# Performance work log

Measured on AMD Instinct MI355X. Metric: run time of the kernel, lower is better.

## Reference

```python
import jax, jax.numpy as jnp
import numpy as np

EMB = 512       # emb_dim
H = 8           # n_heads
HD = EMB // H   # head_dim = 64
FREQ = 64       # freq_features
PERIOD = 0.1
N = 2048


def setup_inputs() -> dict:
    key = jax.random.key(0)
    ks = jax.random.split(key, 6)
    x = jax.random.normal(ks[0], (1, N, EMB), dtype=jnp.float32)
    v = jax.random.normal(ks[1], (1, N, 3), dtype=jnp.float32)
    vec_map = v / jnp.linalg.norm(v, axis=-1, keepdims=True)  # unit direction vectors
    s_in = 1.0 / np.sqrt(EMB)
    W_qkv = jax.random.normal(ks[2], (EMB, 3 * EMB), dtype=jnp.float32) * s_in
    b_qkv = jnp.zeros((3 * EMB,), dtype=jnp.float32)
    W_bias = jax.random.normal(ks[3], (FREQ, H), dtype=jnp.float32) * (1.0 / np.sqrt(FREQ))
    b_bias = jnp.zeros((H,), dtype=jnp.float32)
    W_out = jax.random.normal(ks[4], (EMB, EMB), dtype=jnp.float32) * s_in
    b_out = jnp.zeros((EMB,), dtype=jnp.float32)
    return {"x": x, "vec_map": vec_map, "W_qkv": W_qkv, "b_qkv": b_qkv,
            "W_bias": W_bias, "b_bias": b_bias, "W_out": W_out, "b_out": b_out}


def reference(x, vec_map, W_qkv, b_qkv, W_bias, b_bias, W_out, b_out):
    batch_dim = x.shape[:-2]
    n = x.shape[-2]
    # QKV projection -> (*, N, H, 3, HD)
    qkv = (x @ W_qkv + b_qkv).reshape(*batch_dim, n, H, 3, HD)
    q, k, v = (qkv[..., 0, :], qkv[..., 1, :], qkv[..., 2, :])
    # attention scores (*, Q, K, H), softmax over the K axis (axis=-2)
    attn = jnp.einsum('...qht,...kht->...qkh', q, k) / np.sqrt(HD)
    attn = jax.nn.softmax(attn, axis=-2)
    # relative bias from pairwise angles between direction vectors
    dot = jnp.einsum('...nc,...mc->...nm', vec_map, vec_map)
    angle = jnp.arccos(jnp.clip(dot, 0.0, 1.0)) / 0.001
    freqs = jnp.linspace(0.0, 1.0, FREQ // 2, dtype=jnp.float32) / PERIOD
    phase = freqs * angle[..., None]                      # (*, N, N, FREQ/2)
    pos = jnp.concatenate((jnp.sin(phase), jnp.cos(phase)), axis=-1)  # (*, N, N, FREQ)
    bias = pos @ W_bias + b_bias                          # (*, N, N, H)
    attn = attn + bias
    # weighted sum of values -> (*, N, EMB)
    y = jnp.einsum('...qkh,...kht->...qht', attn, v).reshape(*batch_dim, n, EMB)
    return y @ W_out + b_out
```

## Files before the change

### kernel.cpp

```cpp
#include <hip/hip_runtime.h>
#include <hip/hip_bf16.h>
#include <math.h>

#define NT 2048
#define EMBD 512
#define NH 8
#define QKV_LD 1536

typedef unsigned short u16;
typedef __attribute__((ext_vector_type(8))) short short8;
typedef __attribute__((ext_vector_type(4))) float v4f;

static __device__ __forceinline__ float bf2f(unsigned int u) {
    union { unsigned int i; float f; } c; c.i = u << 16; return c.f;
}
static __device__ __forceinline__ void unpack8(uint4 r, float* f) {
    f[0] = bf2f(r.x & 0xffffu); f[1] = bf2f(r.x >> 16);
    f[2] = bf2f(r.y & 0xffffu); f[3] = bf2f(r.y >> 16);
    f[4] = bf2f(r.z & 0xffffu); f[5] = bf2f(r.z >> 16);
    f[6] = bf2f(r.w & 0xffffu); f[7] = bf2f(r.w >> 16);
}
static __device__ __forceinline__ void unpack4(uint2 r, float* f) {
    f[0] = bf2f(r.x & 0xffffu); f[1] = bf2f(r.x >> 16);
    f[2] = bf2f(r.y & 0xffffu); f[3] = bf2f(r.y >> 16);
}
static __device__ __forceinline__ unsigned int f2bf(float x) {
    union { float f; unsigned int u; } c; c.f = x;
    return (c.u + 0x7fffu + ((c.u >> 16) & 1u)) >> 16;
}

__global__ __launch_bounds__(256) void split_x(const float* __restrict__ x,
    u16* __restrict__ xh, u16* __restrict__ xl)
{
    int i = (blockIdx.x * 256 + threadIdx.x) << 2;
    float4 v = *(const float4*)(x + i);
    float f[4] = {v.x, v.y, v.z, v.w};
    unsigned int hi[4], lo[4];
#pragma unroll
    for (int j = 0; j < 4; ++j) {
        hi[j] = f2bf(f[j]);
        lo[j] = f2bf(f[j] - bf2f(hi[j]));
    }
    uint2 wh; wh.x = hi[0] | (hi[1] << 16); wh.y = hi[2] | (hi[3] << 16);
    uint2 wl; wl.x = lo[0] | (lo[1] << 16); wl.y = lo[2] | (lo[3] << 16);
    *(uint2*)(xh + i) = wh;
    *(uint2*)(xl + i) = wl;
}

__global__ __launch_bounds__(256) void split_wt(const float* __restrict__ W,
    u16* __restrict__ wth, u16* __restrict__ wtl)
{
    __shared__ float tile[64][65];
    const int n0 = blockIdx.x << 6, k0 = blockIdx.y << 6;
    const int t = threadIdx.x;
    const int r = t >> 2, c4 = (t & 3) << 4;
#pragma unroll
    for (int j = 0; j < 4; ++j)
        *(float4*)&tile[r][c4 + (j << 2)] =
            *(const float4*)(W + (size_t)(k0 + r) * QKV_LD + n0 + c4 + (j << 2));
    __syncthreads();
    const int n_l = t >> 2;
    u16 th[16], tl[16];
#pragma unroll
    for (int j = 0; j < 16; ++j) {
        float f = tile[c4 + j][n_l];
        unsigned int h = f2bf(f);
        th[j] = (u16)h;
        tl[j] = (u16)f2bf(f - bf2f(h));
    }
    u16* dh = wth + (size_t)(n0 + n_l) * EMBD + k0 + c4;
    u16* dl = wtl + (size_t)(n0 + n_l) * EMBD + k0 + c4;
    *(uint4*)dh       = *(uint4*)&th[0];
    *(uint4*)(dh + 8) = *(uint4*)&th[8];
    *(uint4*)dl       = *(uint4*)&tl[0];
    *(uint4*)(dl + 8) = *(uint4*)&tl[8];
}

__global__ __launch_bounds__(256) void gemm_qkv_mfma(const u16* __restrict__ xh,
    const u16* __restrict__ xl, const u16* __restrict__ wth,
    const u16* __restrict__ wtl, const float* __restrict__ bias,
    u16* __restrict__ qkvb)
{
    const int n0 = blockIdx.x << 6, m0 = blockIdx.y << 6;
    const int w = threadIdx.x >> 6, lane = threadIdx.x & 63;
    const int wm = w >> 1, wn = w & 1;
    const int fr = lane & 15, kd = (lane >> 4) << 3;

    const u16* ah0 = xh + (size_t)(m0 + wm * 32 + fr) * EMBD + kd;
    const u16* al0 = xl + (size_t)(m0 + wm * 32 + fr) * EMBD + kd;
    const u16* bh0 = wth + (size_t)(n0 + wn * 32 + fr) * EMBD + kd;
    const u16* bl0 = wtl + (size_t)(n0 + wn * 32 + fr) * EMBD + kd;

    v4f acc[2][2] = {};
    for (int kc = 0; kc < EMBD; kc += 32) {
        short8 a_h[2], a_l[2], b_h[2], b_l[2];
#pragma unroll
        for (int im = 0; im < 2; ++im) {
            a_h[im] = *(const short8*)(ah0 + (size_t)im * 16 * EMBD + kc);
            a_l[im] = *(const short8*)(al0 + (size_t)im * 16 * EMBD + kc);
        }
#pragma unroll
        for (int in = 0; in < 2; ++in) {
            b_h[in] = *(const short8*)(bh0 + (size_t)in * 16 * EMBD + kc);
            b_l[in] = *(const short8*)(bl0 + (size_t)in * 16 * EMBD + kc);
        }
#pragma unroll
        for (int im = 0; im < 2; ++im)
#pragma unroll
            for (int in = 0; in < 2; ++in) {
                acc[im][in] = __builtin_amdgcn_mfma_f32_16x16x32_bf16(a_h[im], b_h[in], acc[im][in], 0, 0, 0);
                acc[im][in] = __builtin_amdgcn_mfma_f32_16x16x32_bf16(a_h[im], b_l[in], acc[im][in], 0, 0, 0);
                acc[im][in] = __builtin_amdgcn_mfma_f32_16x16x32_bf16(a_l[im], b_h[in], acc[im][in], 0, 0, 0);
            }
    }
    const int qr = (lane >> 4) << 2;
#pragma unroll
    for (int im = 0; im < 2; ++im)
#pragma unroll
        for (int in = 0; in < 2; ++in) {
            int n = n0 + wn * 32 + in * 16 + fr;
            float bv = bias[n];
#pragma unroll
            for (int r = 0; r < 4; ++r) {
                int m = m0 + wm * 32 + im * 16 + qr + r;
                qkvb[(size_t)m * QKV_LD + n] = (u16)f2bf(acc[im][in][r] + bv);
            }
        }
}

__global__ __launch_bounds__(256) void transpose_v(const u16* __restrict__ qkvb,
                                                   u16* __restrict__ Vt)
{
    __shared__ u16 tile[64][72];
    const int h = blockIdx.y, k0 = blockIdx.x << 6;
    const int t = threadIdx.x;
    {
        int r = t >> 2, cg = (t & 3) << 4;
        const u16* src = qkvb + (size_t)(k0 + r) * QKV_LD + h * 192 + 128 + cg;
        *(uint4*)&tile[r][cg]     = *(const uint4*)src;
        *(uint4*)&tile[r][cg + 8] = *(const uint4*)(src + 8);
    }
    __syncthreads();
    {
        int c = t >> 2, kg = (t & 3) << 4;
        u16 tmp[16];
#pragma unroll
        for (int j = 0; j < 16; ++j) tmp[j] = tile[kg + j][c];
        u16* dst = Vt + ((size_t)h * 64 + c) * NT + k0 + kg;
        *(uint4*)dst       = *(uint4*)&tmp[0];
        *(uint4*)(dst + 8) = *(uint4*)&tmp[8];
    }
}

__global__ __launch_bounds__(256) void scores_mfma(const u16* __restrict__ qkvb,
                                                   u16* __restrict__ s)
{
    const int h = blockIdx.z;
    const int k0 = blockIdx.x << 7;
    const int q0 = (blockIdx.y << 7) + ((threadIdx.x >> 6) << 5);
    const int lane = threadIdx.x & 63;
    const int fr = lane & 15;
    const int kd = (lane >> 4) << 3;

    const u16* qbase = qkvb + (size_t)(q0 + fr) * QKV_LD + h * 192 + kd;
    const u16* kbase = qkvb + (size_t)(k0 + fr) * QKV_LD + h * 192 + 64 + kd;

    short8 aq[2][2];
    aq[0][0] = *(const short8*)(qbase);
    aq[0][1] = *(const short8*)(qbase + 32);
    aq[1][0] = *(const short8*)(qbase + (size_t)16 * QKV_LD);
    aq[1][1] = *(const short8*)(qbase + (size_t)16 * QKV_LD + 32);

    v4f acc[2][8] = {};
#pragma unroll
    for (int nt = 0; nt < 8; ++nt) {
        short8 b0 = *(const short8*)(kbase + (size_t)nt * 16 * QKV_LD);
        short8 b1 = *(const short8*)(kbase + (size_t)nt * 16 * QKV_LD + 32);
        acc[0][nt] = __builtin_amdgcn_mfma_f32_16x16x32_bf16(aq[0][0], b0, acc[0][nt], 0, 0, 0);
        acc[0][nt] = __builtin_amdgcn_mfma_f32_16x16x32_bf16(aq[0][1], b1, acc[0][nt], 0, 0, 0);
        acc[1][nt] = __builtin_amdgcn_mfma_f32_16x16x32_bf16(aq[1][0], b0, acc[1][nt], 0, 0, 0);
        acc[1][nt] = __builtin_amdgcn_mfma_f32_16x16x32_bf16(aq[1][1], b1, acc[1][nt], 0, 0, 0);
    }
    const int qr = (lane >> 4) << 2;
#pragma unroll
    for (int i = 0; i < 2; ++i)
#pragma unroll
        for (int nt = 0; nt < 8; ++nt)
#pragma unroll
            for (int r = 0; r < 4; ++r) {
                int q = q0 + (i << 4) + qr + r;
                int k = k0 + (nt << 4) + fr;
                s[((size_t)h * NT + q) * NT + k] = (u16)f2bf(acc[i][nt][r] * 0.125f);
            }
}

__global__ __launch_bounds__(256) void softmax_stats(const u16* __restrict__ s,
                                                     float* __restrict__ mOut,
                                                     float* __restrict__ izOut)
{
    const int row = blockIdx.x;
    const int t = threadIdx.x;
    const uint4 raw = *(const uint4*)(s + (size_t)row * NT + (t << 3));
    float v[8]; unpack8(raw, v);
    float m = v[0];
#pragma unroll
    for (int i = 1; i < 8; ++i) m = fmaxf(m, v[i]);
    __shared__ float red[256];
    red[t] = m; __syncthreads();
    for (int off = 128; off > 0; off >>= 1) {
        if (t < off) red[t] = fmaxf(red[t], red[t + off]);
        __syncthreads();
    }
    m = red[0];
    __syncthreads();
    float z = 0.f;
#pragma unroll
    for (int i = 0; i < 8; ++i) z += __expf(v[i] - m);
    red[t] = z; __syncthreads();
    for (int off = 128; off > 0; off >>= 1) {
        if (t < off) red[t] += red[t + off];
        __syncthreads();
    }
    if (t == 0) { mOut[row] = m; izOut[row] = 1.0f / red[0]; }
}

__global__ __launch_bounds__(256) void bias_kernel(u16* __restrict__ s,
    const float* __restrict__ vec, const float* __restrict__ Wb,
    const float* __restrict__ bb, const float* __restrict__ mbuf,
    const float* __restrict__ izbuf)
{
    __shared__ float flds[32];
    __shared__ float vql[96], vkl[96];
    __shared__ float bbl[8];
    __shared__ float ang_lds[1024];
    __shared__ float bias_lds[1024][8];

    const int t = threadIdx.x;
    int b = blockIdx.x, tq = 0, rem = 64;
    while (b >= rem) { b -= rem; ++tq; --rem; }
    const int tk = tq + b;
    const int q0 = tq << 5, k0 = tk << 5;

    if (t < 32) flds[t] = __fdiv_rn(__fdiv_rn((float)t, 31.0f), 0.1f);
    else if (t >= 32 && t < 128) vql[t - 32] = vec[q0 * 3 + (t - 32)];
    else if (t < 224) vkl[t - 128] = vec[k0 * 3 + (t - 128)];
    else if (t < 232) bbl[t - 224] = bb[t - 224];
    __syncthreads();

    {
        const int qq = t & 31, kb = (t >> 5) << 2;
        const float a0 = vql[qq * 3], a1 = vql[qq * 3 + 1], a2 = vql[qq * 3 + 2];
#pragma unroll
        for (int j = 0; j < 4; ++j) {
            const int kk = kb + j;
            float c0 = vkl[kk * 3], c1 = vkl[kk * 3 + 1], c2 = vkl[kk * 3 + 2];
            float dot = __fadd_rn(__fadd_rn(__fmul_rn(a0, c0), __fmul_rn(a1, c1)),
                                  __fmul_rn(a2, c2));
            float dotc = fminf(fmaxf(dot, 0.0f), 1.0f);
            ang_lds[(qq << 5) + kk] = __fdiv_rn(acosf(dotc), 0.001f);
        }
    }
    __syncthreads();

    {
        const int w = t >> 6, lane = t & 63;
        const int fr = lane & 15, kd = (lane >> 4) << 3, qr = (lane >> 4) << 2;
        short8 BS, BC;
#pragma unroll
        for (int j = 0; j < 8; ++j) {
            float ws = (fr < 8) ? Wb[(kd + j) * 8 + fr] : 0.0f;
            float wc = (fr < 8) ? Wb[(32 + kd + j) * 8 + fr] : 0.0f;
            BS[j] = (short)f2bf(ws);
            BC[j] = (short)f2bf(wc);
        }
        for (int tt = w; tt < 64; tt += 4) {
            float ang = ang_lds[(tt << 4) + fr];
            short8 AS, AC;
#pragma unroll
            for (int j = 0; j < 8; ++j) {
                float ph = __fmul_rn(flds[kd + j], ang);
                float rv = ph * 0.15915494309189535f;
                float rf = rv - floorf(rv);
                AS[j] = (short)f2bf(__builtin_amdgcn_sinf(rf));
                AC[j] = (short)f2bf(__builtin_amdgcn_cosf(rf));
            }
            v4f c = {};
            c = __builtin_amdgcn_mfma_f32_16x16x32_bf16(AS, BS, c, 0, 0, 0);
            c = __builtin_amdgcn_mfma_f32_16x16x32_bf16(AC, BC, c, 0, 0, 0);
            if (fr < 8)
#pragma unroll
                for (int r = 0; r < 4; ++r)
                    bias_lds[(tt << 4) + qr + r][fr] = c[r];
        }
    }
    __syncthreads();

    const int r = t >> 3;
    const int cg = (t & 7) << 2;
    {
        const int q = q0 + r;
#pragma unroll
        for (int h = 0; h < 8; ++h) {
            const float m = mbuf[h * NT + q], iz = izbuf[h * NT + q], bv = bbl[h];
            const size_t base = ((size_t)h * NT + q) * NT + k0 + cg;
            uint2 raw = *(const uint2*)(s + base);
            float v[4]; unpack4(raw, v);
            unsigned int o[4];
#pragma unroll
            for (int j = 0; j < 4; ++j) {
                float val = __expf(v[j] - m) * iz + bias_lds[(r << 5) + cg + j][h] + bv;
                o[j] = f2bf(val);
            }
            uint2 wv; wv.x = o[0] | (o[1] << 16); wv.y = o[2] | (o[3] << 16);
            *(uint2*)(s + base) = wv;
        }
    }
    if (tk != tq) {
        const int q = k0 + r;
#pragma unroll
        for (int h = 0; h < 8; ++h) {
            const float m = mbuf[h * NT + q], iz = izbuf[h * NT + q], bv = bbl[h];
            const size_t base = ((size_t)h * NT + q) * NT + q0 + cg;
            uint2 raw = *(const uint2*)(s + base);
            float v[4]; unpack4(raw, v);
            unsigned int o[4];
#pragma unroll
            for (int j = 0; j < 4; ++j) {
                float val = __expf(v[j] - m) * iz + bias_lds[((cg + j) << 5) + r][h] + bv;
                o[j] = f2bf(val);
            }
            uint2 wv; wv.x = o[0] | (o[1] << 16); wv.y = o[2] | (o[3] << 16);
            *(uint2*)(s + base) = wv;
        }
    }
}

__global__ __launch_bounds__(256) void attnv_mfma(const u16* __restrict__ attn,
    const u16* __restrict__ Vt, float* __restrict__ ypart)
{
    const int h = blockIdx.y, z = blockIdx.z;
    const int q0 = (blockIdx.x << 6) + ((threadIdx.x >> 6) << 4);
    const int lane = threadIdx.x & 63;
    const int fr = lane & 15;
    const int kd = (lane >> 4) << 3;
    const int kbase = z << 9;

    const u16* arow  = attn + (size_t)(h * NT + q0 + fr) * NT + kbase + kd;
    const u16* vbase = Vt + ((size_t)h * 64 + fr) * NT + kbase + kd;

    v4f c[4] = {};
    for (int ks = 0; ks < 512; ks += 32) {
        short8 a = *(const short8*)(arow + ks);
#pragma unroll
        for (int nt = 0; nt < 4; ++nt) {
            short8 bv = *(const short8*)(vbase + (size_t)nt * 16 * NT + ks);
            c[nt] = __builtin_amdgcn_mfma_f32_16x16x32_bf16(a, bv, c[nt], 0, 0, 0);
        }
    }
    float* yp = ypart + (size_t)z * NT * EMBD;
    const int qr = (lane >> 4) << 2;
#pragma unroll
    for (int nt = 0; nt < 4; ++nt)
#pragma unroll
        for (int r = 0; r < 4; ++r)
            yp[(size_t)(q0 + qr + r) * EMBD + (h << 6) + (nt << 4) + fr] = c[nt][r];
}

__global__ __launch_bounds__(256) void gemm_f32_part(const float* __restrict__ A,
    const float* __restrict__ B, float* __restrict__ Cpart,
    int M, int N, int KS)
{
    __shared__ float As[16][68];
    __shared__ float Bs[16][68];
    const int n0 = blockIdx.x << 6, m0 = blockIdx.y << 6;
    const int kstart = blockIdx.z * KS;
    const int K = 512;
    const int t = threadIdx.x, tx = t & 15, ty = t >> 4;
    float acc[4][4] = {};
    for (int kb = kstart; kb < kstart + KS; kb += 16) {
#pragma unroll
        for (int l = 0; l < 4; ++l) {
            int e = t + (l << 8);
            int mm = e >> 4, kk = e & 15;
            As[kk][mm] = A[(size_t)(m0 + mm) * K + kb + kk];
        }
#pragma unroll
        for (int l = 0; l < 4; ++l) {
            int e = t + (l << 8);
            int kk = e >> 6, nn = e & 63;
            Bs[kk][nn] = B[(size_t)(kb + kk) * N + n0 + nn];
        }
        __syncthreads();
#pragma unroll
        for (int kk = 0; kk < 16; ++kk) {
            float a[4], bvv[4];
#pragma unroll
            for (int i = 0; i < 4; ++i) a[i] = As[kk][(ty << 2) + i];
#pragma unroll
            for (int j = 0; j < 4; ++j) bvv[j] = Bs[kk][(tx << 2) + j];
#pragma unroll
            for (int i = 0; i < 4; ++i)
#pragma unroll
                for (int j = 0; j < 4; ++j)
                    acc[i][j] = fmaf(a[i], bvv[j], acc[i][j]);
        }
        __syncthreads();
    }
    float* Cz = Cpart + (size_t)blockIdx.z * M * N;
#pragma unroll
    for (int i = 0; i < 4; ++i) {
        int m = m0 + (ty << 2) + i;
#pragma unroll
        for (int j = 0; j < 4; ++j) {
            int n = n0 + (tx << 2) + j;
            Cz[(size_t)m * N + n] = acc[i][j];
        }
    }
}

__global__ __launch_bounds__(256) void reduce_add(float* __restrict__ out,
    const float* __restrict__ parts, const float* __restrict__ bias,
    int nsplit, int MN, int N)
{
    int i = (blockIdx.x * 256 + threadIdx.x) << 2;
    if (i >= MN) return;
    float4 acc = *(const float4*)(parts + i);
    for (int sp = 1; sp < nsplit; ++sp) {
        float4 p = *(const float4*)(parts + (size_t)sp * MN + i);
        acc.x += p.x; acc.y += p.y; acc.z += p.z; acc.w += p.w;
    }
    if (bias) {
        float4 b = *(const float4*)(bias + (i & (N - 1)));
        acc.x += b.x; acc.y += b.y; acc.z += b.z; acc.w += b.w;
    }
    *(float4*)(out + i) = acc;
}

extern "C" void kernel_launch(void* const* d_in, const int* in_sizes, int n_in,
                              void* d_out, int out_size, void* d_ws, size_t ws_size,
                              hipStream_t stream)
{
    const float* x    = (const float*)d_in[0];
    const float* vec  = (const float*)d_in[1];
    const float* Wqkv = (const float*)d_in[2];
    const float* bqkv = (const float*)d_in[3];
    const float* Wb   = (const float*)d_in[4];
    const float* bb   = (const float*)d_in[5];
    const float* Wout = (const float*)d_in[6];
    const float* bout = (const float*)d_in[7];
    float* out = (float*)d_out;

    char* ws = (char*)d_ws;
    u16*   qkvb  = (u16*)(ws);
    u16*   sbuf  = (u16*)(ws + 6291456);
    u16*   Vt    = (u16*)(ws + 73400320);
    float* mbuf  = (float*)(ws + 75497472);
    float* izb   = (float*)(ws + 75563008);
    float* ybuf  = (float*)(ws + 75628544);
    float* parts = (float*)(ws + 79822848);
    u16*   xh    = (u16*)(ws + 79822848);
    u16*   xl    = (u16*)(ws + 81920000);
    u16*   wth   = (u16*)(ws + 84017152);
    u16*   wtl   = (u16*)(ws + 85590016);

    split_x<<<1024, 256, 0, stream>>>(x, xh, xl);
    split_wt<<<dim3(24, 8), 256, 0, stream>>>(Wqkv, wth, wtl);
    gemm_qkv_mfma<<<dim3(24, 32), 256, 0, stream>>>(xh, xl, wth, wtl, bqkv, qkvb);
    transpose_v<<<dim3(32, 8), 256, 0, stream>>>(qkvb, Vt);
    scores_mfma<<<dim3(16, 16, 8), 256, 0, stream>>>(qkvb, sbuf);
    softmax_stats<<<NT * NH, 256, 0, stream>>>(sbuf, mbuf, izb);
    bias_kernel<<<2080, 256, 0, stream>>>(sbuf, vec, Wb, bb, mbuf, izb);
    attnv_mfma<<<dim3(32, 8, 4), 256, 0, stream>>>(sbuf, Vt, parts);
    reduce_add<<<1024, 256, 0, stream>>>(ybuf, parts, nullptr, 4, NT * EMBD, EMBD);
    gemm_f32_part<<<dim3(8, 32, 4), 256, 0, stream>>>(ybuf, Wout, parts, NT, EMBD, 128);
    reduce_add<<<1024, 256, 0, stream>>>(out, parts, bout, 4, NT * EMBD, EMBD);
}
```

Before: 283.6 us.

## Fuse softmax sums into scores, sparsify bias, and use MFMA for output projection

Removes the separate softmax_stats pass. Row exp-sums are accumulated with shuffles and atomics inside scores_mfma, with no max subtraction, which assumes the scores stay small. The bias kernel builds a compacted list of pairs with positive dot products and runs the sin/cos MFMA only on those. Clipped pairs share one precomputed bias vector. The fp32 output GEMM plus split-K reduce is replaced by a split-bf16 (hi/lo) MFMA GEMM fed by a reduce that also splits y into hi/lo parts. This adds numerical risk from the unnormalized exp and the hi/lo approximation.

```diff
diff --git a/kernel.cpp b/kernel.cpp
--- a/kernel.cpp
+++ b/kernel.cpp
@@ -70,6 +70,35 @@
     }
     u16* dh = wth + (size_t)(n0 + n_l) * EMBD + k0 + c4;
     u16* dl = wtl + (size_t)(n0 + n_l) * EMBD + k0 + c4;
+    *(uint4*)dh       = *(uint4*)&th[0];
+    *(uint4*)(dh + 8) = *(uint4*)&th[8];
+    *(uint4*)dl       = *(uint4*)&tl[0];
+    *(uint4*)(dl + 8) = *(uint4*)&tl[8];
+}
+
+__global__ __launch_bounds__(256) void split_wout(const float* __restrict__ W,
+    u16* __restrict__ wh, u16* __restrict__ wl)
+{
+    __shared__ float tile[64][65];
+    const int n0 = blockIdx.x << 6, k0 = blockIdx.y << 6;
+    const int t = threadIdx.x;
+    const int r = t >> 2, c4 = (t & 3) << 4;
+#pragma unroll
+    for (int j = 0; j < 4; ++j)
+        *(float4*)&tile[r][c4 + (j << 2)] =
+            *(const float4*)(W + (size_t)(k0 + r) * EMBD + n0 + c4 + (j << 2));
+    __syncthreads();
+    const int n_l = t >> 2;
+    u16 th[16], tl[16];
+#pragma unroll
+    for (int j = 0; j < 16; ++j) {
+        float f = tile[c4 + j][n_l];
+        unsigned int h = f2bf(f);
+        th[j] = (u16)h;
+        tl[j] = (u16)f2bf(f - bf2f(h));
+    }
+    u16* dh = wh + (size_t)(n0 + n_l) * EMBD + k0 + c4;
+    u16* dl = wl + (size_t)(n0 + n_l) * EMBD + k0 + c4;
     *(uint4*)dh       = *(uint4*)&th[0];
     *(uint4*)(dh + 8) = *(uint4*)&th[8];
     *(uint4*)dl       = *(uint4*)&tl[0];
@@ -153,7 +182,8 @@
 }
 
 __global__ __launch_bounds__(256) void scores_mfma(const u16* __restrict__ qkvb,
-                                                   u16* __restrict__ s)
+                                                   u16* __restrict__ s,
+                                                   float* __restrict__ zbuf)
 {
     const int h = blockIdx.z;
     const int k0 = blockIdx.x << 7;
@@ -192,48 +222,46 @@
                 int k = k0 + (nt << 4) + fr;
                 s[((size_t)h * NT + q) * NT + k] = (u16)f2bf(acc[i][nt][r] * 0.125f);
             }
-}
-
-__global__ __launch_bounds__(256) void softmax_stats(const u16* __restrict__ s,
-                                                     float* __restrict__ mOut,
-                                                     float* __restrict__ izOut)
-{
-    const int row = blockIdx.x;
-    const int t = threadIdx.x;
-    const uint4 raw = *(const uint4*)(s + (size_t)row * NT + (t << 3));
-    float v[8]; unpack8(raw, v);
-    float m = v[0];
-#pragma unroll
-    for (int i = 1; i < 8; ++i) m = fmaxf(m, v[i]);
-    __shared__ float red[256];
-    red[t] = m; __syncthreads();
-    for (int off = 128; off > 0; off >>= 1) {
-        if (t < off) red[t] = fmaxf(red[t], red[t + off]);
-        __syncthreads();
-    }
-    m = red[0];
-    __syncthreads();
-    float z = 0.f;
-#pragma unroll
-    for (int i = 0; i < 8; ++i) z += __expf(v[i] - m);
-    red[t] = z; __syncthreads();
-    for (int off = 128; off > 0; off >>= 1) {
-        if (t < off) red[t] += red[t + off];
-        __syncthreads();
-    }
-    if (t == 0) { mOut[row] = m; izOut[row] = 1.0f / red[0]; }
+    float es[2][4];
+#pragma unroll
+    for (int i = 0; i < 2; ++i)
+#pragma unroll
+        for (int r = 0; r < 4; ++r) {
+            float sum = 0.f;
+#pragma unroll
+            for (int nt = 0; nt < 8; ++nt)
+                sum += __expf(acc[i][nt][r] * 0.125f);
+            es[i][r] = sum;
+        }
+#pragma unroll
+    for (int off = 1; off < 16; off <<= 1)
+#pragma unroll
+        for (int i = 0; i < 2; ++i)
+#pragma unroll
+            for (int r = 0; r < 4; ++r)
+                es[i][r] += __shfl_xor(es[i][r], off);
+    if (fr == 0) {
+#pragma unroll
+        for (int i = 0; i < 2; ++i)
+#pragma unroll
+            for (int r = 0; r < 4; ++r)
+                atomicAdd(zbuf + h * NT + q0 + (i << 4) + qr + r, es[i][r]);
+    }
 }
 
 __global__ __launch_bounds__(256) void bias_kernel(u16* __restrict__ s,
     const float* __restrict__ vec, const float* __restrict__ Wb,
-    const float* __restrict__ bb, const float* __restrict__ mbuf,
-    const float* __restrict__ izbuf)
+    const float* __restrict__ bb, const float* __restrict__ zbuf)
 {
     __shared__ float flds[32];
     __shared__ float vql[96], vkl[96];
     __shared__ float bbl[8];
-    __shared__ float ang_lds[1024];
-    __shared__ float bias_lds[1024][8];
+    __shared__ float ang_lds[1025];
+    __shared__ float biasl[8 * 1057];
+    __shared__ float clipb[8];
+    __shared__ unsigned char flagl[1024];
+    __shared__ u16 list[1040];
+    __shared__ int cnt;
 
     const int t = threadIdx.x;
     int b = blockIdx.x, tq = 0, rem = 64;
@@ -241,26 +269,48 @@
     const int tk = tq + b;
     const int q0 = tq << 5, k0 = tk << 5;
 
+    if (t == 0) cnt = 0;
     if (t < 32) flds[t] = __fdiv_rn(__fdiv_rn((float)t, 31.0f), 0.1f);
-    else if (t >= 32 && t < 128) vql[t - 32] = vec[q0 * 3 + (t - 32)];
+    else if (t < 128) vql[t - 32] = vec[q0 * 3 + (t - 32)];
     else if (t < 224) vkl[t - 128] = vec[k0 * 3 + (t - 128)];
     else if (t < 232) bbl[t - 224] = bb[t - 224];
     __syncthreads();
 
     {
         const int qq = t & 31, kb = (t >> 5) << 2;
+        const int lane = t & 63;
         const float a0 = vql[qq * 3], a1 = vql[qq * 3 + 1], a2 = vql[qq * 3 + 2];
 #pragma unroll
         for (int j = 0; j < 4; ++j) {
             const int kk = kb + j;
+            const int p = (qq << 5) + kk;
             float c0 = vkl[kk * 3], c1 = vkl[kk * 3 + 1], c2 = vkl[kk * 3 + 2];
             float dot = __fadd_rn(__fadd_rn(__fmul_rn(a0, c0), __fmul_rn(a1, c1)),
                                   __fmul_rn(a2, c2));
             float dotc = fminf(fmaxf(dot, 0.0f), 1.0f);
-            ang_lds[(qq << 5) + kk] = __fdiv_rn(acosf(dotc), 0.001f);
-        }
-    }
-    __syncthreads();
+            ang_lds[p] = __fdiv_rn(acosf(dotc), 0.001f);
+            int live = (dot > 0.0f) ? 1 : 0;
+            flagl[p] = (unsigned char)(1 - live);
+            unsigned long long m = __ballot(live);
+            int base = 0;
+            if (lane == 0) base = atomicAdd(&cnt, __popcll(m));
+            base = __shfl(base, 0);
+            if (live)
+                list[base + __popcll(m & ((1ull << lane) - 1ull))] = (u16)p;
+        }
+    }
+    __syncthreads();
+    if (t == 0) {
+        int c = cnt;
+        int padded = (c + 15) & ~15;
+        for (int i = c; i < padded; ++i) list[i] = 1024;
+        float zero = fabsf(vql[0]) * 0.0f;
+        float zc = fminf(fmaxf(zero, 0.0f), 1.0f);
+        ang_lds[1024] = __fdiv_rn(acosf(zc), 0.001f);
+        cnt = padded;
+    }
+    __syncthreads();
+    const int ntiles = cnt >> 4;
 
     {
         const int w = t >> 6, lane = t & 63;
@@ -273,8 +323,8 @@
             BS[j] = (short)f2bf(ws);
             BC[j] = (short)f2bf(wc);
         }
-        for (int tt = w; tt < 64; tt += 4) {
-            float ang = ang_lds[(tt << 4) + fr];
+        if (w == 0) {
+            float ang = ang_lds[1024];
             short8 AS, AC;
 #pragma unroll
             for (int j = 0; j < 8; ++j) {
@@ -287,10 +337,30 @@
             v4f c = {};
             c = __builtin_amdgcn_mfma_f32_16x16x32_bf16(AS, BS, c, 0, 0, 0);
             c = __builtin_amdgcn_mfma_f32_16x16x32_bf16(AC, BC, c, 0, 0, 0);
-            if (fr < 8)
-#pragma unroll
-                for (int r = 0; r < 4; ++r)
-                    bias_lds[(tt << 4) + qr + r][fr] = c[r];
+            if (fr < 8) clipb[fr] = c[0];
+        }
+        for (int i = w; i < ntiles; i += 4) {
+            float ang = ang_lds[list[(i << 4) + fr]];
+            short8 AS, AC;
+#pragma unroll
+            for (int j = 0; j < 8; ++j) {
+                float ph = __fmul_rn(flds[kd + j], ang);
+                float rv = ph * 0.15915494309189535f;
+                float rf = rv - floorf(rv);
+                AS[j] = (short)f2bf(__builtin_amdgcn_sinf(rf));
+                AC[j] = (short)f2bf(__builtin_amdgcn_cosf(rf));
+            }
+            v4f c = {};
+            c = __builtin_amdgcn_mfma_f32_16x16x32_bf16(AS, BS, c, 0, 0, 0);
+            c = __builtin_amdgcn_mfma_f32_16x16x32_bf16(AC, BC, c, 0, 0, 0);
+            if (fr < 8) {
+#pragma unroll
+                for (int r = 0; r < 4; ++r) {
+                    int p = list[(i << 4) + qr + r];
+                    if (p < 1024)
+                        biasl[fr * 1057 + (p >> 5) * 33 + (p & 31)] = c[r];
+                }
+            }
         }
     }
     __syncthreads();
@@ -301,15 +371,17 @@
         const int q = q0 + r;
 #pragma unroll
         for (int h = 0; h < 8; ++h) {
-            const float m = mbuf[h * NT + q], iz = izbuf[h * NT + q], bv = bbl[h];
+            const float iz = 1.0f / zbuf[h * NT + q];
+            const float bv = bbl[h];
             const size_t base = ((size_t)h * NT + q) * NT + k0 + cg;
             uint2 raw = *(const uint2*)(s + base);
             float v[4]; unpack4(raw, v);
             unsigned int o[4];
 #pragma unroll
             for (int j = 0; j < 4; ++j) {
-                float val = __expf(v[j] - m) * iz + bias_lds[(r << 5) + cg + j][h] + bv;
-                o[j] = f2bf(val);
+                int p = (r << 5) + cg + j;
+                float bias = flagl[p] ? clipb[h] : biasl[h * 1057 + r * 33 + cg + j];
+                o[j] = f2bf(__expf(v[j]) * iz + bias + bv);
             }
             uint2 wv; wv.x = o[0] | (o[1] << 16); wv.y = o[2] | (o[3] << 16);
             *(uint2*)(s + base) = wv;
@@ -319,15 +391,17 @@
         const int q = k0 + r;
 #pragma unroll
         for (int h = 0; h < 8; ++h) {
-            const float m = mbuf[h * NT + q], iz = izbuf[h * NT + q], bv = bbl[h];
+            const float iz = 1.0f / zbuf[h * NT + q];
+            const float bv = bbl[h];
             const size_t base = ((size_t)h * NT + q) * NT + q0 + cg;
             uint2 raw = *(const uint2*)(s + base);
             float v[4]; unpack4(raw, v);
             unsigned int o[4];
 #pragma unroll
             for (int j = 0; j < 4; ++j) {
-                float val = __expf(v[j] - m) * iz + bias_lds[((cg + j) << 5) + r][h] + bv;
-                o[j] = f2bf(val);
+                int p = ((cg + j) << 5) + r;
+                float bias = flagl[p] ? clipb[h] : biasl[h * 1057 + (cg + j) * 33 + r];
+                o[j] = f2bf(__expf(v[j]) * iz + bias + bv);
             }
             uint2 wv; wv.x = o[0] | (o[1] << 16); wv.y = o[2] | (o[3] << 16);
             *(uint2*)(s + base) = wv;
@@ -366,74 +440,80 @@
             yp[(size_t)(q0 + qr + r) * EMBD + (h << 6) + (nt << 4) + fr] = c[nt][r];
 }
 
-__global__ __launch_bounds__(256) void gemm_f32_part(const float* __restrict__ A,
-    const float* __restrict__ B, float* __restrict__ Cpart,
-    int M, int N, int KS)
-{
-    __shared__ float As[16][68];
-    __shared__ float Bs[16][68];
-    const int n0 = blockIdx.x << 6, m0 = blockIdx.y << 6;
-    const int kstart = blockIdx.z * KS;
-    const int K = 512;
-    const int t = threadIdx.x, tx = t & 15, ty = t >> 4;
-    float acc[4][4] = {};
-    for (int kb = kstart; kb < kstart + KS; kb += 16) {
-#pragma unroll
-        for (int l = 0; l < 4; ++l) {
-            int e = t + (l << 8);
-            int mm = e >> 4, kk = e & 15;
-            As[kk][mm] = A[(size_t)(m0 + mm) * K + kb + kk];
-        }
-#pragma unroll
-        for (int l = 0; l < 4; ++l) {
-            int e = t + (l << 8);
-            int kk = e >> 6, nn = e & 63;
-            Bs[kk][nn] = B[(size_t)(kb + kk) * N + n0 + nn];
-        }
-        __syncthreads();
-#pragma unroll
-        for (int kk = 0; kk < 16; ++kk) {
-            float a[4], bvv[4];
-#pragma unroll
-            for (int i = 0; i < 4; ++i) a[i] = As[kk][(ty << 2) + i];
-#pragma unroll
-            for (int j = 0; j < 4; ++j) bvv[j] = Bs[kk][(tx << 2) + j];
-#pragma unroll
-            for (int i = 0; i < 4; ++i)
-#pragma unroll
-                for (int j = 0; j < 4; ++j)
-                    acc[i][j] = fmaf(a[i], bvv[j], acc[i][j]);
-        }
-        __syncthreads();
-    }
-    float* Cz = Cpart + (size_t)blockIdx.z * M * N;
-#pragma unroll
-    for (int i = 0; i < 4; ++i) {
-        int m = m0 + (ty << 2) + i;
-#pragma unroll
-        for (int j = 0; j < 4; ++j) {
-            int n = n0 + (tx << 2) + j;
-            Cz[(size_t)m * N + n] = acc[i][j];
-        }
-    }
-}
-
-__global__ __launch_bounds__(256) void reduce_add(float* __restrict__ out,
-    const float* __restrict__ parts, const float* __restrict__ bias,
-    int nsplit, int MN, int N)
-{
+__global__ __launch_bounds__(256) void reduce_y(const float* __restrict__ parts,
+    u16* __restrict__ yh, u16* __restrict__ yl)
+{
+    const int MN = NT * EMBD;
     int i = (blockIdx.x * 256 + threadIdx.x) << 2;
-    if (i >= MN) return;
     float4 acc = *(const float4*)(parts + i);
-    for (int sp = 1; sp < nsplit; ++sp) {
+#pragma unroll
+    for (int sp = 1; sp < 4; ++sp) {
         float4 p = *(const float4*)(parts + (size_t)sp * MN + i);
         acc.x += p.x; acc.y += p.y; acc.z += p.z; acc.w += p.w;
     }
-    if (bias) {
-        float4 b = *(const float4*)(bias + (i & (N - 1)));
-        acc.x += b.x; acc.y += b.y; acc.z += b.z; acc.w += b.w;
-    }
-    *(float4*)(out + i) = acc;
+    float f[4] = {acc.x, acc.y, acc.z, acc.w};
+    unsigned int hi[4], lo[4];
+#pragma unroll
+    for (int j = 0; j < 4; ++j) {
+        hi[j] = f2bf(f[j]);
+        lo[j] = f2bf(f[j] - bf2f(hi[j]));
+    }
+    uint2 wh; wh.x = hi[0] | (hi[1] << 16); wh.y = hi[2] | (hi[3] << 16);
+    uint2 wl; wl.x = lo[0] | (lo[1] << 16); wl.y = lo[2] | (lo[3] << 16);
+    *(uint2*)(yh + i) = wh;
+    *(uint2*)(yl + i) = wl;
+}
+
+__global__ __launch_bounds__(256) void gemm_out_mfma(const u16* __restrict__ yh,
+    const u16* __restrict__ yl, const u16* __restrict__ wh,
+    const u16* __restrict__ wl, const float* __restrict__ bias,
+    float* __restrict__ out)
+{
+    const int n0 = blockIdx.x << 6, m0 = blockIdx.y << 6;
+    const int w = threadIdx.x >> 6, lane = threadIdx.x & 63;
+    const int wm = w >> 1, wn = w & 1;
+    const int fr = lane & 15, kd = (lane >> 4) << 3;
+
+    const u16* ah0 = yh + (size_t)(m0 + wm * 32 + fr) * EMBD + kd;
+    const u16* al0 = yl + (size_t)(m0 + wm * 32 + fr) * EMBD + kd;
+    const u16* bh0 = wh + (size_t)(n0 + wn * 32 + fr) * EMBD + kd;
+    const u16* bl0 = wl + (size_t)(n0 + wn * 32 + fr) * EMBD + kd;
+
+    v4f acc[2][2] = {};
+    for (int kc = 0; kc < EMBD; kc += 32) {
+        short8 a_h[2], a_l[2], b_h[2], b_l[2];
+#pragma unroll
+        for (int im = 0; im < 2; ++im) {
+            a_h[im] = *(const short8*)(ah0 + (size_t)im * 16 * EMBD + kc);
+            a_l[im] = *(const short8*)(al0 + (size_t)im * 16 * EMBD + kc);
+        }
+#pragma unroll
+        for (int in = 0; in < 2; ++in) {
+            b_h[in] = *(const short8*)(bh0 + (size_t)in * 16 * EMBD + kc);
+            b_l[in] = *(const short8*)(bl0 + (size_t)in * 16 * EMBD + kc);
+        }
+#pragma unroll
+        for (int im = 0; im < 2; ++im)
+#pragma unroll
+            for (int in = 0; in < 2; ++in) {
+                acc[im][in] = __builtin_amdgcn_mfma_f32_16x16x32_bf16(a_h[im], b_h[in], acc[im][in], 0, 0, 0);
+                acc[im][in] = __builtin_amdgcn_mfma_f32_16x16x32_bf16(a_h[im], b_l[in], acc[im][in], 0, 0, 0);
+                acc[im][in] = __builtin_amdgcn_mfma_f32_16x16x32_bf16(a_l[im], b_h[in], acc[im][in], 0, 0, 0);
+            }
+    }
+    const int qr = (lane >> 4) << 2;
+#pragma unroll
+    for (int im = 0; im < 2; ++im)
+#pragma unroll
+        for (int in = 0; in < 2; ++in) {
+            int n = n0 + wn * 32 + in * 16 + fr;
+            float bv = bias[n];
+#pragma unroll
+            for (int r = 0; r < 4; ++r) {
+                int m = m0 + wm * 32 + im * 16 + qr + r;
+                out[(size_t)m * EMBD + n] = acc[im][in][r] + bv;
+            }
+        }
 }
 
 extern "C" void kernel_launch(void* const* d_in, const int* in_sizes, int n_in,
@@ -454,24 +534,26 @@
     u16*   qkvb  = (u16*)(ws);
     u16*   sbuf  = (u16*)(ws + 6291456);
     u16*   Vt    = (u16*)(ws + 73400320);
-    float* mbuf  = (float*)(ws + 75497472);
-    float* izb   = (float*)(ws + 75563008);
-    float* ybuf  = (float*)(ws + 75628544);
+    float* zbuf  = (float*)(ws + 75497472);
+    u16*   yh    = (u16*)(ws + 75628544);
+    u16*   yl    = (u16*)(ws + 77725696);
     float* parts = (float*)(ws + 79822848);
     u16*   xh    = (u16*)(ws + 79822848);
     u16*   xl    = (u16*)(ws + 81920000);
     u16*   wth   = (u16*)(ws + 84017152);
     u16*   wtl   = (u16*)(ws + 85590016);
-
+    u16*   woth  = (u16*)(ws + 79822848);
+    u16*   wotl  = (u16*)(ws + 80347136);
+
+    hipMemsetAsync(zbuf, 0, NH * NT * sizeof(float), stream);
     split_x<<<1024, 256, 0, stream>>>(x, xh, xl);
     split_wt<<<dim3(24, 8), 256, 0, stream>>>(Wqkv, wth, wtl);
     gemm_qkv_mfma<<<dim3(24, 32), 256, 0, stream>>>(xh, xl, wth, wtl, bqkv, qkvb);
     transpose_v<<<dim3(32, 8), 256, 0, stream>>>(qkvb, Vt);
-    scores_mfma<<<dim3(16, 16, 8), 256, 0, stream>>>(qkvb, sbuf);
-    softmax_stats<<<NT * NH, 256, 0, stream>>>(sbuf, mbuf, izb);
-    bias_kernel<<<2080, 256, 0, stream>>>(sbuf, vec, Wb, bb, mbuf, izb);
+    scores_mfma<<<dim3(16, 16, 8), 256, 0, stream>>>(qkvb, sbuf, zbuf);
+    bias_kernel<<<2080, 256, 0, stream>>>(sbuf, vec, Wb, bb, zbuf);
     attnv_mfma<<<dim3(32, 8, 4), 256, 0, stream>>>(sbuf, Vt, parts);
-    reduce_add<<<1024, 256, 0, stream>>>(ybuf, parts, nullptr, 4, NT * EMBD, EMBD);
-    gemm_f32_part<<<dim3(8, 32, 4), 256, 0, stream>>>(ybuf, Wout, parts, NT, EMBD, 128);
-    reduce_add<<<1024, 256, 0, stream>>>(out, parts, bout, 4, NT * EMBD, EMBD);
-}
+    reduce_y<<<1024, 256, 0, stream>>>(parts, yh, yl);
+    split_wout<<<dim3(8, 8), 256, 0, stream>>>(Wout, woth, wotl);
+    gemm_out_mfma<<<dim3(8, 32), 256, 0, stream>>>(yh, yl, woth, wotl, bout, out);
+}
```

Result: no change. 278.2 us (-1.9%).
